# Kernel tuning notes

Measured on AMD Instinct MI355X. Metric: run time of the kernel, lower is better.

Reference implementation:

```python
import jax, jax.numpy as jnp
import numpy as np

B, N, F_IN, H, C = 256, 512, 14, 30, 2
CLUSTERS = [8, 4, 2, 1]


def _gcn(x, adj, W, b):
    # DenseGCNConv: set diagonal of adj to 1 (self loops), sym-normalize, propagate
    n = adj.shape[-1]
    eye = jnp.eye(n, dtype=adj.dtype)
    a = adj * (1.0 - eye) + eye
    dis = jnp.clip(a.sum(-1), 1.0, None) ** -0.5  # [B, n]
    a = dis[..., :, None] * a * dis[..., None, :]
    return jnp.einsum('bij,bjh->bih', a, x @ W) + b


def _diff_pool(x, adj, W, b):
    # DiffPool module applies softmax over node dim (dim=1), then
    # dense_diff_pool applies softmax over cluster dim (dim=-1)
    s = jax.nn.softmax(x @ W + b, axis=1)
    s = jax.nn.softmax(s, axis=-1)          # [B, n, c]
    xp = jnp.einsum('bnc,bnf->bcf', s, x)
    ap = jnp.einsum('bnc,bnm,bmd->bcd', s, adj, s)
    link = jnp.linalg.norm(adj - jnp.einsum('bnc,bmc->bnm', s, s)) / adj.size
    ent = jnp.mean(jnp.sum(-s * jnp.log(s + 1e-15), axis=-1))
    return xp, ap, link, ent


def _forward(x, adj, cws, cbs, pws, pbs, lw, lb):
    r = jax.nn.relu
    x = r(_gcn(x, adj, cws[0], cbs[0]))
    x = r(_gcn(x, adj, cws[1], cbs[1]))
    x = r(_gcn(x, adj, cws[2], cbs[2]))
    x = _gcn(x, adj, cws[3], cbs[3])        # no relu before first pool
    x, adj, _, _ = _diff_pool(x, adj, pws[0], pbs[0])
    x = r(_gcn(x, adj, cws[4], cbs[4]))
    x, adj, _, _ = _diff_pool(x, adj, pws[1], pbs[1])
    x = r(_gcn(x, adj, cws[5], cbs[5]))
    x, adj, _, _ = _diff_pool(x, adj, pws[2], pbs[2])
    x = r(_gcn(x, adj, cws[6], cbs[6]))
    x, adj, _, _ = _diff_pool(x, adj, pws[3], pbs[3])
    x = r(_gcn(x, adj, cws[7], cbs[7]))     # [B, 1, H]
    return (x @ lw + lb).squeeze()          # [B, C]


def setup_inputs() -> dict:
    key = jax.random.key(0)
    ks = jax.random.split(key, 40)
    inp = {}
    inp['x'] = jax.random.normal(ks[0], (B, N, F_IN), jnp.float32)
    inp['adj'] = (jax.random.uniform(ks[1], (B, N, N)) < 0.05).astype(jnp.float32)
    inp['edge_index'] = jax.random.randint(ks[2], (2, 4096), 0, N, dtype=jnp.int32)
    inp['batch'] = jnp.zeros((B * N,), jnp.int32)
    dims = [(F_IN, H)] + [(H, H)] * 7
    for i, (di, do) in enumerate(dims):
        inp[f'cw{i}'] = jax.random.normal(ks[3 + i], (di, do), jnp.float32) * (di ** -0.5)
        inp[f'cb{i}'] = jnp.zeros((do,), jnp.float32)
    for i, c in enumerate(CLUSTERS):
        inp[f'pw{i}'] = jax.random.normal(ks[12 + i], (H, c), jnp.float32) * (H ** -0.5)
        inp[f'pb{i}'] = jnp.zeros((c,), jnp.float32)
    inp['lw'] = jax.random.normal(ks[20], (H, C), jnp.float32) * (H ** -0.5)
    inp['lb'] = jnp.zeros((C,), jnp.float32)
    return inp


def reference(x, adj, edge_index, batch,
              cw0, cb0, cw1, cb1, cw2, cb2, cw3, cb3,
              cw4, cb4, cw5, cb5, cw6, cb6, cw7, cb7,
              pw0, pb0, pw1, pb1, pw2, pb2, pw3, pb3,
              lw, lb):
    cws = [cw0, cw1, cw2, cw3, cw4, cw5, cw6, cw7]
    cbs = [cb0, cb1, cb2, cb3, cb4, cb5, cb6, cb7]
    pws = [pw0, pw1, pw2, pw3]
    pbs = [pb0, pb1, pb2, pb3]
    return _forward(x, adj, cws, cbs, pws, pbs, lw, lb)
```

## Files before the change

### kernel.cpp

```cpp
#include <hip/hip_runtime.h>
#include <cstdint>
#include <cstddef>

#define B_ 256
#define N_ 512
#define RCAP 72
#define STRX 36

typedef unsigned short u16;

constexpr size_t O_COLIDX = 0;
constexpr size_t O_ROWCNT = 18874368;
constexpr size_t O_DIS    = 19398656;
constexpr size_t O_DIAG   = 19922944;

__global__ __launch_bounds__(256) void build_sparse(
    const float* __restrict__ adj, u16* __restrict__ colidx,
    int* __restrict__ rowcnt, float* __restrict__ dis, float* __restrict__ diagv)
{
    int row  = blockIdx.x * 4 + (threadIdx.x >> 6);
    int lane = threadIdx.x & 63;
    int i    = row & (N_ - 1);
    const float4* arow = (const float4*)(adj + (size_t)row * N_);
    float4 v0 = arow[lane];
    float4 v1 = arow[lane + 64];
    float vals[8] = {v0.x, v0.y, v0.z, v0.w, v1.x, v1.y, v1.z, v1.w};

    float sum = 0.f, dloc = 0.f;
    int cnt = 0;
    #pragma unroll
    for (int k = 0; k < 8; ++k) {
        int jc = (k < 4) ? (lane * 4 + k) : (256 + lane * 4 + (k - 4));
        float v = vals[k];
        if (jc == i) dloc = v;
        else { sum += v; if (v != 0.f) ++cnt; }
    }
    int pre = cnt;
    #pragma unroll
    for (int d = 1; d < 64; d <<= 1) { int y = __shfl_up(pre, d, 64); if (lane >= d) pre += y; }
    int excl  = pre - cnt;
    int total = __shfl(pre, 63, 64);
    #pragma unroll
    for (int d = 32; d > 0; d >>= 1) { sum += __shfl_xor(sum, d, 64); dloc += __shfl_xor(dloc, d, 64); }

    u16* cb = colidx + (size_t)row * RCAP;
    int c2 = 0;
    #pragma unroll
    for (int k = 0; k < 8; ++k) {
        int jc = (k < 4) ? (lane * 4 + k) : (256 + lane * 4 + (k - 4));
        float v = vals[k];
        if (jc != i && v != 0.f) { int p = excl + c2; if (p < RCAP) cb[p] = (u16)jc; ++c2; }
    }
    int base = total > RCAP ? RCAP : total;
    int p1 = base + lane;      if (p1 < RCAP) cb[p1] = (u16)N_;
    int p2 = base + 64 + lane; if (p2 < RCAP) cb[p2] = (u16)N_;
    if (lane == 0) {
        rowcnt[row] = (base + 7) >> 3;
        dis[row]    = rsqrtf(fmaxf(1.f, sum + 1.f));
        diagv[row]  = dloc;
    }
}

template <int FIN, bool RELU>
__device__ __forceinline__ void glayer(
    int n, int hf, float di, int nch, const u16* __restrict__ cidx_n,
    float* __restrict__ XA, float* __restrict__ XB,
    const float* __restrict__ W, const float* __restrict__ Bs, float* xr)
{
    float acc[16];
    #pragma unroll
    for (int h = 0; h < 16; ++h) acc[h] = 0.f;
    if (hf == 0) {
        #pragma unroll
        for (int f = 0; f < FIN; ++f) {
            float xv = xr[f];
            #pragma unroll
            for (int h = 0; h < 16; ++h) acc[h] = fmaf(xv, W[f * 30 + h], acc[h]);
        }
    } else {
        #pragma unroll
        for (int f = 0; f < FIN; ++f) {
            float xv = xr[f];
            #pragma unroll
            for (int h = 0; h < 14; ++h) acc[h] = fmaf(xv, W[f * 30 + 16 + h], acc[h]);
        }
    }
    #pragma unroll
    for (int h = 0; h < 16; ++h) acc[h] *= di;
    int ho = hf * 16;
    #pragma unroll
    for (int d = 0; d < 4; ++d)
        *(float4*)&XA[n * STRX + ho + 4 * d] =
            make_float4(acc[4*d], acc[4*d+1], acc[4*d+2], acc[4*d+3]);
    __syncthreads();

    for (int ch = 0; ch < nch; ++ch) {
        uint4 cw = *(const uint4*)(cidx_n + ch * 8);
        int j0 = (int)(cw.x & 0xffffu), j1 = (int)(cw.x >> 16);
        int j2 = (int)(cw.y & 0xffffu), j3 = (int)(cw.y >> 16);
        int j4 = (int)(cw.z & 0xffffu), j5 = (int)(cw.z >> 16);
        int j6 = (int)(cw.w & 0xffffu), j7 = (int)(cw.w >> 16);
        #define ACCROW(JJ) { const float* rp = &XA[(JJ) * STRX + ho]; \
            _Pragma("unroll") for (int d = 0; d < 4; ++d) { \
                const float4 v = *(const float4*)&rp[4 * d]; \
                acc[4*d+0] += v.x; acc[4*d+1] += v.y; \
                acc[4*d+2] += v.z; acc[4*d+3] += v.w; } }
        ACCROW(j0) ACCROW(j1) ACCROW(j2) ACCROW(j3)
        ACCROW(j4) ACCROW(j5) ACCROW(j6) ACCROW(j7)
        #undef ACCROW
    }
    float rr[16];
    if (hf == 0) {
        #pragma unroll
        for (int h = 0; h < 16; ++h) {
            float r = fmaf(di, acc[h], Bs[h]);
            rr[h] = RELU ? fmaxf(r, 0.f) : r;
        }
    } else {
        #pragma unroll
        for (int h = 0; h < 14; ++h) {
            float r = fmaf(di, acc[h], Bs[16 + h]);
            rr[h] = RELU ? fmaxf(r, 0.f) : r;
        }
        rr[14] = 0.f; rr[15] = 0.f;
    }
    #pragma unroll
    for (int d = 0; d < 4; ++d)
        *(float4*)&XB[n * STRX + ho + 4 * d] =
            make_float4(rr[4*d], rr[4*d+1], rr[4*d+2], rr[4*d+3]);
    __syncthreads();

    if (hf == 0) {
        #pragma unroll
        for (int h = 0; h < 16; ++h) xr[h] = rr[h];
        #pragma unroll
        for (int d = 0; d < 4; ++d) {
            const float4 v = *(const float4*)&XB[n * STRX + 16 + 4 * d];
            if (d < 3) { xr[16+4*d] = v.x; xr[17+4*d] = v.y; xr[18+4*d] = v.z; xr[19+4*d] = v.w; }
            else       { xr[28] = v.x; xr[29] = v.y; }
        }
    } else {
        #pragma unroll
        for (int h = 0; h < 14; ++h) xr[16 + h] = rr[h];
        #pragma unroll
        for (int d = 0; d < 4; ++d) {
            const float4 v = *(const float4*)&XB[n * STRX + 4 * d];
            xr[4*d] = v.x; xr[4*d+1] = v.y; xr[4*d+2] = v.z; xr[4*d+3] = v.w;
        }
    }
}

__device__ void gcn_small(int n, int t, const float* X, float* XN, float* XW, float* DIS,
                          const float* A, const float* W, const float* Bias, bool relu)
{
    if (t < n) {
        float s = 1.f;
        for (int jj = 0; jj < n; ++jj) if (jj != t) s += A[t * 8 + jj];
        DIS[t] = rsqrtf(fmaxf(1.f, s));
    }
    __syncthreads();
    if (t < n * 30) {
        int i = t / 30, h = t - i * 30;
        float acc = 0.f;
        #pragma unroll
        for (int f = 0; f < 30; ++f) acc += X[i * 30 + f] * W[f * 30 + h];
        XW[t] = acc * DIS[i];
    }
    __syncthreads();
    if (t < n * 30) {
        int i = t / 30, h = t - i * 30;
        float acc = XW[i * 30 + h];
        for (int jj = 0; jj < n; ++jj) if (jj != i) acc += A[i * 8 + jj] * XW[jj * 30 + h];
        float r = DIS[i] * acc + Bias[h];
        if (relu) r = fmaxf(r, 0.f);
        XN[t] = r;
    }
    __syncthreads();
}

__device__ void pool_small(int n, int c, int t, const float* X, const float* A,
                           const float* PW, const float* PB,
                           float* S, float* T, float* LG, float* XN, float* AN)
{
    if (t < n * c) {
        int i = t / c, k = t - i * c;
        float acc = PB[k];
        #pragma unroll
        for (int h = 0; h < 30; ++h) acc += X[i * 30 + h] * PW[h * c + k];
        LG[i * 8 + k] = acc;
    }
    __syncthreads();
    if (t < c) {
        float mx = -1e30f;
        for (int i = 0; i < n; ++i) mx = fmaxf(mx, LG[i * 8 + t]);
        float sm = 0.f;
        for (int i = 0; i < n; ++i) { float e = __expf(LG[i * 8 + t] - mx); LG[i * 8 + t] = e; sm += e; }
        float inv = 1.f / sm;
        for (int i = 0; i < n; ++i) LG[i * 8 + t] *= inv;
    }
    __syncthreads();
    if (t < n) {
        float mx = -1e30f;
        for (int k = 0; k < c; ++k) mx = fmaxf(mx, LG[t * 8 + k]);
        float sm = 0.f;
        for (int k = 0; k < c; ++k) { float e = __expf(LG[t * 8 + k] - mx); S[t * 8 + k] = e; sm += e; }
        float inv = 1.f / sm;
        for (int k = 0; k < c; ++k) S[t * 8 + k] *= inv;
    }
    __syncthreads();
    if (t < c * 30) {
        int k = t / 30, f = t - k * 30;
        float acc = 0.f;
        for (int i = 0; i < n; ++i) acc += S[i * 8 + k] * X[i * 30 + f];
        XN[t] = acc;
    }
    if (t < n * c) {
        int i = t / c, d = t - i * c;
        float acc = 0.f;
        for (int m = 0; m < n; ++m) acc += A[i * 8 + m] * S[m * 8 + d];
        T[i * 8 + d] = acc;
    }
    __syncthreads();
    if (t < c * c) {
        int k = t / c, d = t - k * c;
        float acc = 0.f;
        for (int i = 0; i < n; ++i) acc += S[i * 8 + k] * T[i * 8 + d];
        AN[k * 8 + d] = acc;
    }
    __syncthreads();
}

__global__ __launch_bounds__(1024) void mega6_kernel(
    const float* __restrict__ x0,
    const float* __restrict__ W0, const float* __restrict__ Bs0,
    const float* __restrict__ W1, const float* __restrict__ Bs1,
    const float* __restrict__ W2, const float* __restrict__ Bs2,
    const float* __restrict__ W3, const float* __restrict__ Bs3,
    const float* __restrict__ pw, const float* __restrict__ pb,
    const float* cw4, const float* cb4, const float* cw5, const float* cb5,
    const float* cw6, const float* cb6, const float* cw7, const float* cb7,
    const float* pw1, const float* pb1, const float* pw2, const float* pb2,
    const float* pw3, const float* pb3, const float* lw, const float* lb,
    const u16* __restrict__ colidx, const int* __restrict__ rowcnt,
    const float* __restrict__ dis, const float* __restrict__ diagv,
    float* __restrict__ out)
{
    __shared__ __align__(16) float XA[(N_ + 1) * STRX];
    __shared__ __align__(16) float XB[(N_ + 1) * STRX];
    __shared__ float bufX[240], bufY[240], TXW[240], TDIS[8];
    __shared__ float bufA[64], bufB[64], TS[64], TT[64], TLG[64];

    const int b = blockIdx.x, t = threadIdx.x;
    const int n = t & (N_ - 1), hf = t >> 9;

    const u16* cidx_n = colidx + ((size_t)b * N_ + n) * RCAP;
    int   nch = rowcnt[(size_t)b * N_ + n];
    float di  = dis  [(size_t)b * N_ + n];
    float dg  = diagv[(size_t)b * N_ + n];
    if (t < STRX) XA[N_ * STRX + t] = 0.f;

    float xr[30];
    {
        const float2* xrow = (const float2*)(x0 + ((size_t)b * N_ + n) * 14);
        #pragma unroll
        for (int k = 0; k < 7; ++k) { float2 v = xrow[k]; xr[2*k] = v.x; xr[2*k+1] = v.y; }
    }

    glayer<14, true >(n, hf, di, nch, cidx_n, XA, XB, W0, Bs0, xr);
    glayer<30, true >(n, hf, di, nch, cidx_n, XA, XB, W1, Bs1, xr);
    glayer<30, true >(n, hf, di, nch, cidx_n, XA, XB, W2, Bs2, xr);
    glayer<30, false>(n, hf, di, nch, cidx_n, XA, XB, W3, Bs3, xr);

    float* ls   = XA;
    float* ltp  = XA + 6156;
    float* red  = XA + 12300;
    float* red2 = XA + 16396;

    {
        int c0 = hf * 4;
        float lg[4];
        #pragma unroll
        for (int c = 0; c < 4; ++c) lg[c] = pb[c0 + c];
        #pragma unroll
        for (int h = 0; h < 30; ++h) {
            float xv = xr[h];
            #pragma unroll
            for (int c = 0; c < 4; ++c) lg[c] = fmaf(xv, pw[h * 8 + c0 + c], lg[c]);
        }
        *(float4*)&ls[n * 12 + c0] = make_float4(lg[0], lg[1], lg[2], lg[3]);
        if (t < 12) ls[N_ * 12 + t] = 0.f;
    }
    __syncthreads();
    if (t < 512) {
        int c = t >> 6, lane = t & 63;
        float v[8]; float mx = -1e30f;
        #pragma unroll
        for (int k = 0; k < 8; ++k) { v[k] = ls[(k * 64 + lane) * 12 + c]; mx = fmaxf(mx, v[k]); }
        #pragma unroll
        for (int d = 32; d > 0; d >>= 1) mx = fmaxf(mx, __shfl_xor(mx, d, 64));
        float sm = 0.f;
        #pragma unroll
        for (int k = 0; k < 8; ++k) { v[k] = __expf(v[k] - mx); sm += v[k]; }
        #pragma unroll
        for (int d = 32; d > 0; d >>= 1) sm += __shfl_xor(sm, d, 64);
        float inv = 1.f / sm;
        #pragma unroll
        for (int k = 0; k < 8; ++k) ls[(k * 64 + lane) * 12 + c] = v[k] * inv;
    }
    __syncthreads();
    if (t < 512) {
        float v[8]; float mx = -1e30f;
        #pragma unroll
        for (int c = 0; c < 8; ++c) { v[c] = ls[t * 12 + c]; mx = fmaxf(mx, v[c]); }
        float sm = 0.f;
        #pragma unroll
        for (int c = 0; c < 8; ++c) { v[c] = __expf(v[c] - mx); sm += v[c]; }
        float inv = 1.f / sm;
        *(float4*)&ls[t * 12]     = make_float4(v[0]*inv, v[1]*inv, v[2]*inv, v[3]*inv);
        *(float4*)&ls[t * 12 + 4] = make_float4(v[4]*inv, v[5]*inv, v[6]*inv, v[7]*inv);
    }
    __syncthreads();
    {
        int d0 = hf * 4;
        const float4 sown = *(const float4*)&ls[n * 12 + d0];
        float a0 = dg * sown.x, a1 = dg * sown.y, a2 = dg * sown.z, a3 = dg * sown.w;
        for (int ch = 0; ch < nch; ++ch) {
            uint4 cw = *(const uint4*)(cidx_n + ch * 8);
            #define LTROW(JJ) { const float4 u0 = *(const float4*)&ls[(JJ) * 12 + d0]; \
                                a0 += u0.x; a1 += u0.y; a2 += u0.z; a3 += u0.w; }
            LTROW((int)(cw.x & 0xffffu)) LTROW((int)(cw.x >> 16))
            LTROW((int)(cw.y & 0xffffu)) LTROW((int)(cw.y >> 16))
            LTROW((int)(cw.z & 0xffffu)) LTROW((int)(cw.z >> 16))
            LTROW((int)(cw.w & 0xffffu)) LTROW((int)(cw.w >> 16))
            #undef LTROW
        }
        *(float4*)&ltp[n * 12 + d0] = make_float4(a0, a1, a2, a3);
    }
    __syncthreads();
    {
        int seg = t >> 6, cd = t & 63, c = cd >> 3, dd = cd & 7;
        float a0 = 0.f, a1 = 0.f, a2 = 0.f, a3 = 0.f;
        for (int nn = seg * 32; nn < seg * 32 + 32; ++nn) {
            float sv = ls[nn * 12 + c];
            const float4 xv = *(const float4*)&XB[nn * STRX + 4 * dd];
            a0 = fmaf(sv, xv.x, a0); a1 = fmaf(sv, xv.y, a1);
            a2 = fmaf(sv, xv.z, a2); a3 = fmaf(sv, xv.w, a3);
        }
        *(float4*)&red[t * 4] = make_float4(a0, a1, a2, a3);
    }
    {
        int seg = t >> 6, c = (t >> 3) & 7, d = t & 7;
        float s1 = 0.f;
        for (int nn = seg * 32; nn < seg * 32 + 32; ++nn)
            s1 = fmaf(ls[nn * 12 + c], ltp[nn * 12 + d], s1);
        red2[t] = s1;
    }
    __syncthreads();
    if (t < 240) {
        int c = t / 30, f = t - c * 30, dd = f >> 2, m = f & 3;
        float s1 = 0.f;
        #pragma unroll
        for (int seg = 0; seg < 16; ++seg) s1 += red[(seg * 64 + c * 8 + dd) * 4 + m];
        bufX[t] = s1;
    } else if (t >= 256 && t < 320) {
        int tt = t - 256;
        float s1 = 0.f;
        #pragma unroll
        for (int seg = 0; seg < 16; ++seg) s1 += red2[seg * 64 + tt];
        bufA[tt] = s1;
    }
    __syncthreads();

    float *X = bufX, *XN = bufY, *A = bufA, *AN = bufB;
    gcn_small(8, t, X, XN, TXW, TDIS, A, cw4, cb4, true);    { float* tm = X; X = XN; XN = tm; }
    pool_small(8, 4, t, X, A, pw1, pb1, TS, TT, TLG, XN, AN); { float* tm = X; X = XN; XN = tm; tm = A; A = AN; AN = tm; }
    gcn_small(4, t, X, XN, TXW, TDIS, A, cw5, cb5, true);    { float* tm = X; X = XN; XN = tm; }
    pool_small(4, 2, t, X, A, pw2, pb2, TS, TT, TLG, XN, AN); { float* tm = X; X = XN; XN = tm; tm = A; A = AN; AN = tm; }
    gcn_small(2, t, X, XN, TXW, TDIS, A, cw6, cb6, true);    { float* tm = X; X = XN; XN = tm; }
    pool_small(2, 1, t, X, A, pw3, pb3, TS, TT, TLG, XN, AN); { float* tm = X; X = XN; XN = tm; tm = A; A = AN; AN = tm; }
    gcn_small(1, t, X, XN, TXW, TDIS, A, cw7, cb7, true);    { float* tm = X; X = XN; XN = tm; }

    if (t < 2) {
        float acc = lb[t];
        #pragma unroll
        for (int h = 0; h < 30; ++h) acc += X[h] * lw[h * 2 + t];
        out[(size_t)b * 2 + t] = acc;
    }
}

extern "C" void kernel_launch(void* const* d_in, const int* in_sizes, int n_in,
                              void* d_out, int out_size, void* d_ws, size_t ws_size,
                              hipStream_t stream)
{
    const float* x   = (const float*)d_in[0];
    const float* adj = (const float*)d_in[1];
    const float *cw[8], *cb[8], *pw[4], *pb[4];
    for (int i = 0; i < 8; ++i) { cw[i] = (const float*)d_in[4 + 2 * i]; cb[i] = (const float*)d_in[5 + 2 * i]; }
    for (int i = 0; i < 4; ++i) { pw[i] = (const float*)d_in[20 + 2 * i]; pb[i] = (const float*)d_in[21 + 2 * i]; }
    const float* lw = (const float*)d_in[28];
    const float* lb = (const float*)d_in[29];

    char* ws = (char*)d_ws;
    u16*   colidx = (u16*)(ws + O_COLIDX);
    int*   rowcnt = (int*)(ws + O_ROWCNT);
    float* dis0   = (float*)(ws + O_DIS);
    float* diag0  = (float*)(ws + O_DIAG);

    build_sparse<<<(B_ * N_) / 4, 256, 0, stream>>>(adj, colidx, rowcnt, dis0, diag0);
    mega6_kernel<<<B_, 1024, 0, stream>>>(x,
        cw[0], cb[0], cw[1], cb[1], cw[2], cb[2], cw[3], cb[3],
        pw[0], pb[0],
        cw[4], cb[4], cw[5], cb[5], cw[6], cb[6], cw[7], cb[7],
        pw[1], pb[1], pw[2], pb[2], pw[3], pb[3], lw, lb,
        colidx, rowcnt, dis0, diag0, (float*)d_out);
}
```

Measured before the change: 140.2 us.

## Store GCN neighbor features as bf16 in shared memory to halve gather bytes

The per-layer scaled features that neighbors gather from shared memory are now packed as bf16 pairs (row stride 40 halves) instead of fp32, so each neighbor row read is two 16-byte loads instead of four. Accumulation stays in fp32 via bit-shift unpacking. The smaller XA buffer forces the diff-pool scratch reductions into a new SC shared array and compacts the ltp layout to stride 8. This trades precision (bf16 rounding of messages) for lower LDS bandwidth in the sparse gather, and changes total shared memory use.

```diff
diff --git a/kernel.cpp b/kernel.cpp
--- a/kernel.cpp
+++ b/kernel.cpp
@@ -6,6 +6,7 @@
 #define N_ 512
 #define RCAP 72
 #define STRX 36
+#define SBH  40
 
 typedef unsigned short u16;
 
@@ -61,10 +62,19 @@
     }
 }
 
+__device__ __forceinline__ float blo(unsigned u) { return __uint_as_float(u << 16); }
+__device__ __forceinline__ float bhi(unsigned u) { return __uint_as_float(u & 0xffff0000u); }
+__device__ __forceinline__ unsigned pk2(float a, float b) {
+    unsigned ua = __float_as_uint(a), ub = __float_as_uint(b);
+    ua = (ua + 0x7fffu + ((ua >> 16) & 1u)) >> 16;
+    ub = (ub + 0x7fffu + ((ub >> 16) & 1u)) & 0xffff0000u;
+    return ua | ub;
+}
+
 template <int FIN, bool RELU>
 __device__ __forceinline__ void glayer(
     int n, int hf, float di, int nch, const u16* __restrict__ cidx_n,
-    float* __restrict__ XA, float* __restrict__ XB,
+    u16* __restrict__ XA, float* __restrict__ XB,
     const float* __restrict__ W, const float* __restrict__ Bs, float* xr)
 {
     float acc[16];
@@ -87,11 +97,11 @@
     }
     #pragma unroll
     for (int h = 0; h < 16; ++h) acc[h] *= di;
-    int ho = hf * 16;
-    #pragma unroll
-    for (int d = 0; d < 4; ++d)
-        *(float4*)&XA[n * STRX + ho + 4 * d] =
-            make_float4(acc[4*d], acc[4*d+1], acc[4*d+2], acc[4*d+3]);
+    const int ho = hf * 16;
+    *(uint4*)&XA[n * SBH + ho] =
+        make_uint4(pk2(acc[0],acc[1]), pk2(acc[2],acc[3]), pk2(acc[4],acc[5]), pk2(acc[6],acc[7]));
+    *(uint4*)&XA[n * SBH + ho + 8] =
+        make_uint4(pk2(acc[8],acc[9]), pk2(acc[10],acc[11]), pk2(acc[12],acc[13]), pk2(acc[14],acc[15]));
     __syncthreads();
 
     for (int ch = 0; ch < nch; ++ch) {
@@ -100,11 +110,17 @@
         int j2 = (int)(cw.y & 0xffffu), j3 = (int)(cw.y >> 16);
         int j4 = (int)(cw.z & 0xffffu), j5 = (int)(cw.z >> 16);
         int j6 = (int)(cw.w & 0xffffu), j7 = (int)(cw.w >> 16);
-        #define ACCROW(JJ) { const float* rp = &XA[(JJ) * STRX + ho]; \
-            _Pragma("unroll") for (int d = 0; d < 4; ++d) { \
-                const float4 v = *(const float4*)&rp[4 * d]; \
-                acc[4*d+0] += v.x; acc[4*d+1] += v.y; \
-                acc[4*d+2] += v.z; acc[4*d+3] += v.w; } }
+        #define ACCROW(JJ) { \
+            const uint4 v0 = *(const uint4*)&XA[(JJ) * SBH + ho]; \
+            const uint4 v1 = *(const uint4*)&XA[(JJ) * SBH + ho + 8]; \
+            acc[0]  += blo(v0.x); acc[1]  += bhi(v0.x); \
+            acc[2]  += blo(v0.y); acc[3]  += bhi(v0.y); \
+            acc[4]  += blo(v0.z); acc[5]  += bhi(v0.z); \
+            acc[6]  += blo(v0.w); acc[7]  += bhi(v0.w); \
+            acc[8]  += blo(v1.x); acc[9]  += bhi(v1.x); \
+            acc[10] += blo(v1.y); acc[11] += bhi(v1.y); \
+            acc[12] += blo(v1.z); acc[13] += bhi(v1.z); \
+            acc[14] += blo(v1.w); acc[15] += bhi(v1.w); }
         ACCROW(j0) ACCROW(j1) ACCROW(j2) ACCROW(j3)
         ACCROW(j4) ACCROW(j5) ACCROW(j6) ACCROW(j7)
         #undef ACCROW
@@ -230,7 +246,7 @@
     __syncthreads();
 }
 
-__global__ __launch_bounds__(1024) void mega6_kernel(
+__global__ __launch_bounds__(1024) void mega7_kernel(
     const float* __restrict__ x0,
     const float* __restrict__ W0, const float* __restrict__ Bs0,
     const float* __restrict__ W1, const float* __restrict__ Bs1,
@@ -245,8 +261,9 @@
     const float* __restrict__ dis, const float* __restrict__ diagv,
     float* __restrict__ out)
 {
-    __shared__ __align__(16) float XA[(N_ + 1) * STRX];
+    __shared__ __align__(16) u16   XA[(N_ + 1) * SBH];
     __shared__ __align__(16) float XB[(N_ + 1) * STRX];
+    __shared__ __align__(16) float SC[5120];
     __shared__ float bufX[240], bufY[240], TXW[240], TDIS[8];
     __shared__ float bufA[64], bufB[64], TS[64], TT[64], TLG[64];
 
@@ -257,7 +274,7 @@
     int   nch = rowcnt[(size_t)b * N_ + n];
     float di  = dis  [(size_t)b * N_ + n];
     float dg  = diagv[(size_t)b * N_ + n];
-    if (t < STRX) XA[N_ * STRX + t] = 0.f;
+    if (t < 20) ((unsigned*)&XA[N_ * SBH])[t] = 0u;
 
     float xr[30];
     {
@@ -271,10 +288,11 @@
     glayer<30, true >(n, hf, di, nch, cidx_n, XA, XB, W2, Bs2, xr);
     glayer<30, false>(n, hf, di, nch, cidx_n, XA, XB, W3, Bs3, xr);
 
-    float* ls   = XA;
-    float* ltp  = XA + 6156;
-    float* red  = XA + 12300;
-    float* red2 = XA + 16396;
+    float* XAf  = (float*)XA;
+    float* ls   = XAf;
+    float* ltp  = XAf + 6156;
+    float* red  = SC;
+    float* red2 = SC + 4096;
 
     {
         int c0 = hf * 4;
@@ -334,7 +352,7 @@
             LTROW((int)(cw.w & 0xffffu)) LTROW((int)(cw.w >> 16))
             #undef LTROW
         }
-        *(float4*)&ltp[n * 12 + d0] = make_float4(a0, a1, a2, a3);
+        *(float4*)&ltp[n * 8 + d0] = make_float4(a0, a1, a2, a3);
     }
     __syncthreads();
     {
@@ -352,7 +370,7 @@
         int seg = t >> 6, c = (t >> 3) & 7, d = t & 7;
         float s1 = 0.f;
         for (int nn = seg * 32; nn < seg * 32 + 32; ++nn)
-            s1 = fmaf(ls[nn * 12 + c], ltp[nn * 12 + d], s1);
+            s1 = fmaf(ls[nn * 12 + c], ltp[nn * 8 + d], s1);
         red2[t] = s1;
     }
     __syncthreads();
@@ -407,7 +425,7 @@
     float* diag0  = (float*)(ws + O_DIAG);
 
     build_sparse<<<(B_ * N_) / 4, 256, 0, stream>>>(adj, colidx, rowcnt, dis0, diag0);
-    mega6_kernel<<<B_, 1024, 0, stream>>>(x,
+    mega7_kernel<<<B_, 1024, 0, stream>>>(x,
         cw[0], cb[0], cw[1], cb[1], cw[2], cb[2], cw[3], cb[3],
         pw[0], pb[0],
         cw[4], cb[4], cw[5], cb[5], cw[6], cb[6], cw[7], cb[7],
```

After: 226.8 us. +61.8%, slower.
